# Kernel tuning notes

Measured on AMD Instinct MI355X. Metric: run time of the kernel, lower is better.

## Reference

```python
import math
import jax, jax.numpy as jnp
import numpy as np

B, C, F_, W = 4, 2, 512, 1024
NH = 8
HD = F_ // NH            # 64 head dim
ROT = HD // 2            # 32 rotated dims
NFREQ = ROT // 2         # 16 base freqs ('pixel': linspace(1, max_freq/2, dim//2)*pi)


def mc_linear(x, w_pw):
    # x: [b,c,f_in,w], w_pw: [c, f_out, f_in] -> [b,c,f_out,w]
    return jnp.einsum('bchw,cgh->bcgw', x, w_pw)


def apply_rope(t, freqs):
    # t: [b,c,n,w,d]; freqs: [w, rot_dim] (already pair-repeated)
    rot_dim = freqs.shape[-1]
    t_rot, t_pass = t[..., :rot_dim], t[..., rot_dim:]
    cos, sin = jnp.cos(freqs), jnp.sin(freqs)
    x1, x2 = t_rot[..., 0::2], t_rot[..., 1::2]
    rh = jnp.stack([-x2, x1], axis=-1).reshape(t_rot.shape)  # rotate_half (interleaved pairs)
    return jnp.concatenate([t_rot * cos + rh * sin, t_pass], axis=-1)


def setup_inputs() -> dict:
    key = jax.random.key(0)
    ks = jax.random.split(key, 6)
    x = jax.random.normal(ks[0], (B, C, F_, W), dtype=jnp.float32)
    bound = 1.0 / math.sqrt(F_)
    def w(k):
        return jax.random.uniform(k, (C, F_, F_), minval=-bound, maxval=bound, dtype=jnp.float32)
    wq, wk, wv, wo = w(ks[1]), w(ks[2]), w(ks[3]), w(ks[4])
    # learned 'pixel' freqs: linspace(1., max_freq/2=5., NFREQ) * pi
    freqs_param = (jnp.linspace(1.0, 5.0, NFREQ) * math.pi).astype(jnp.float32)
    return {"x": x, "wq": wq, "wk": wk, "wv": wv, "wo": wo, "freqs_param": freqs_param}


def reference(x, wq, wk, wv, wo, freqs_param):
    b, c, h, w = x.shape
    def heads(t):  # [b,c,h,w] -> [b,c,NH,w,HD]
        return t.transpose(0, 1, 3, 2).reshape(b, c, w, NH, HD).transpose(0, 1, 3, 2, 4)
    pos = jnp.arange(w, dtype=jnp.float32)
    freqs = jnp.repeat(pos[:, None] * freqs_param[None, :], 2, axis=-1)  # [w, ROT]
    # NOTE: original module uses q_proj for q, k, and v (k_proj/v_proj unused)
    q = apply_rope(heads(mc_linear(x, wq)), freqs)
    k = apply_rope(heads(mc_linear(x, wq)), freqs)
    v = heads(mc_linear(x, wq))
    qk = jnp.einsum('bcnqd,bcnkd->bcnqk', q, k) / math.sqrt(h)
    a = jnp.einsum('bcnqk,bcnkd->bcnqd', jax.nn.softmax(qk, axis=-1), v)
    a = a.transpose(0, 1, 3, 2, 4).reshape(b, c, w, NH * HD).transpose(0, 1, 3, 2)  # [b,c,h,w]
    return mc_linear(a, wo)
```

## Files before the change

### kernel.cpp

```cpp
#include <hip/hip_runtime.h>
#include <hip/hip_bf16.h>
#include <math.h>

#define B_ 4
#define C_ 2
#define F_ 512
#define W_ 1024
#define NH_ 8
#define HD_ 64
#define ROT_ 32
#define NFREQ_ 16
#define BC_ (B_*C_)

#define QSC_ 0.2525048f

typedef short bf16x8 __attribute__((ext_vector_type(8)));
typedef float f32x4  __attribute__((ext_vector_type(4)));
typedef float f32x16 __attribute__((ext_vector_type(16)));
typedef unsigned short u16;
typedef unsigned int   u32;

#if __has_builtin(__builtin_amdgcn_exp2f)
#define EXP2(x) __builtin_amdgcn_exp2f(x)
#else
#define EXP2(x) exp2f(x)
#endif

#define VDRAIN() asm volatile("s_waitcnt vmcnt(0)" ::: "memory")

__device__ __forceinline__ u16 f2bf(float f) {
    union { float f; u32 u; } v; v.f = f;
    u32 r = (v.u + 0x7fffu + ((v.u >> 16) & 1u)) >> 16;
    return (u16)r;
}
__device__ __forceinline__ float bf2f(u16 h) {
    union { u32 u; float f; } v; v.u = ((u32)h) << 16;
    return v.f;
}
__device__ __forceinline__ f32x4 mfma16(bf16x8 a, bf16x8 b, f32x4 c) {
    return __builtin_amdgcn_mfma_f32_16x16x32_bf16(a, b, c, 0, 0, 0);
}
__device__ __forceinline__ f32x16 mfma32(bf16x8 a, bf16x8 b, f32x16 c) {
    return __builtin_amdgcn_mfma_f32_32x32x16_bf16(a, b, c, 0, 0, 0);
}
__device__ __forceinline__ void gload16(const u16* g, u16* l) {
    __builtin_amdgcn_global_load_lds(
        (const __attribute__((address_space(1))) u32*)g,
        (__attribute__((address_space(3))) u32*)l, 16, 0, 0);
}
__device__ __forceinline__ u32 pk2(float lo, float hi) {
    __hip_bfloat162 h = __float22bfloat162_rn(make_float2(lo, hi));
    union { __hip_bfloat162 b; u32 u; } cv; cv.b = h; return cv.u;
}
__device__ __forceinline__ void pl32swap(u32& a, u32& b) {
    asm volatile("v_permlane32_swap_b32 %0, %1" : "+v"(a), "+v"(b));
}

__global__ __launch_bounds__(256)
void prep(const float* __restrict__ wq, const float* __restrict__ wo,
          const float* __restrict__ fp,
          u16* __restrict__ wqh, u16* __restrict__ woh, u16* __restrict__ wol,
          float2* __restrict__ trig)
{
    const int b = blockIdx.x, t = threadIdx.x;
    if (b < 512) {
        int i = (b * 256 + t) * 4;
        float4 v = *(const float4*)(wq + i);
        ushort4 h;
        h.x = f2bf(v.x); h.y = f2bf(v.y); h.z = f2bf(v.z); h.w = f2bf(v.w);
        *(ushort4*)(wqh + i) = h;
    } else if (b < 1024) {
        int i = ((b - 512) * 256 + t) * 4;
        float4 v = *(const float4*)(wo + i);
        ushort4 h, l;
        h.x = f2bf(v.x); l.x = f2bf(v.x - bf2f(h.x));
        h.y = f2bf(v.y); l.y = f2bf(v.y - bf2f(h.y));
        h.z = f2bf(v.z); l.z = f2bf(v.z - bf2f(h.z));
        h.w = f2bf(v.w); l.w = f2bf(v.w - bf2f(h.w));
        *(ushort4*)(woh + i) = h;
        *(ushort4*)(wol + i) = l;
    } else {
        int idx = (b - 1024) * 256 + t;
        int w = idx >> 4, j = idx & 15;
        float th = (float)w * fp[j];
        float s, c;
        sincosf(th, &s, &c);
        trig[idx] = make_float2(c, s);
    }
}

__global__ __launch_bounds__(256)
void conv_xt(const float* __restrict__ x, u16* __restrict__ xh) {
    __shared__ float T[64][65];
    const int t = threadIdx.x;
    const int h0 = blockIdx.x * 64, w0 = blockIdx.y * 64, bc = blockIdx.z;
    {
        const int hl = t >> 2, wc = (t & 3) * 16;
        const float* src = x + ((size_t)bc * F_ + h0 + hl) * W_ + w0 + wc;
        #pragma unroll
        for (int z = 0; z < 4; ++z)
            *(float4*)(&T[hl][wc + z * 4]) = *(const float4*)(src + z * 4);
    }
    __syncthreads();
    {
        const int wl = t >> 2, hc = (t & 3) * 16;
        u16 hv[16];
        #pragma unroll
        for (int z = 0; z < 16; ++z) hv[z] = f2bf(T[hc + z][wl]);
        size_t base = ((size_t)bc * W_ + w0 + wl) * F_ + h0 + hc;
        *(uint4*)(xh + base)     = *(uint4*)(hv);
        *(uint4*)(xh + base + 8) = *(uint4*)(hv + 8);
    }
}

template<int MODE>
__global__ __launch_bounds__(256)
void gemm3(const u16* __restrict__ Ah_, const u16* __restrict__ Al_,
           const u16* __restrict__ Bh_, const u16* __restrict__ Bl_,
           u16* __restrict__ Vout, u16* __restrict__ Qout,
           float* __restrict__ Fout, const float2* __restrict__ trig)
{
    constexpr int BUFS = MODE ? 16384 : 8192;
    __shared__ u16 sh[2 * BUFS];

    const int tid = threadIdx.x, lane = tid & 63, wid = tid >> 6;
    const int m0 = blockIdx.x * 128, n0 = blockIdx.y * 128, bc = blockIdx.z, c = bc % C_;
    const u16* Abh = Ah_ + (size_t)c * F_ * F_;
    const u16* Abl = MODE ? (Al_ + (size_t)c * F_ * F_) : (const u16*)nullptr;
    const u16* Bbh = Bh_ + (size_t)bc * W_ * F_;
    const u16* Bbl = MODE ? (Bl_ + (size_t)bc * W_ * F_) : (const u16*)nullptr;

    f32x4 acc[4][4] = {};
    const int mb = (wid >> 1) * 64, nb = (wid & 1) * 64;
    const int r_in = lane >> 2, tsl = lane & 3;

    auto STAGE = [&](int k0, int buf) {
        u16* base = sh + buf * BUFS;
        #pragma unroll
        for (int h = 0; h < 2; ++h) {
            const int row = h * 64 + wid * 16 + r_in;
            const int ts  = tsl ^ ((row >> 1) & 3);
            const int lb  = (h * 64 + wid * 16) * 32;
            gload16(Abh + (size_t)(m0 + row) * F_ + k0 + ts * 8, base + lb);
            gload16(Bbh + (size_t)(n0 + row) * F_ + k0 + ts * 8, base + 4096 + lb);
            if constexpr (MODE) {
                gload16(Abl + (size_t)(m0 + row) * F_ + k0 + ts * 8, base + 8192 + lb);
                gload16(Bbl + (size_t)(n0 + row) * F_ + k0 + ts * 8, base + 12288 + lb);
            }
        }
    };

    STAGE(0, 0);
    VDRAIN();
    __syncthreads();
    int cur = 0;
    for (int kt = 0; kt < 16; ++kt) {
        if (kt < 15) STAGE((kt + 1) * 32, cur ^ 1);
        const u16* Ash = sh + cur * BUFS;
        const u16* Bsh = Ash + 4096;
        const u16* Asl = MODE ? Ash + 8192  : Ash;
        const u16* Bsl = MODE ? Ash + 12288 : Ash;

        bf16x8 fah[4], fal[4];
        #pragma unroll
        for (int i = 0; i < 4; ++i) {
            const int row = mb + i * 16 + (lane & 15);
            const int idx = row * 32 + (((lane >> 4) ^ ((row >> 1) & 3)) << 3);
            fah[i] = *(const bf16x8*)(&Ash[idx]);
            if constexpr (MODE) fal[i] = *(const bf16x8*)(&Asl[idx]);
        }
        #pragma unroll
        for (int j = 0; j < 4; ++j) {
            const int rowb = nb + j * 16 + (lane & 15);
            const int idxb = rowb * 32 + (((lane >> 4) ^ ((rowb >> 1) & 3)) << 3);
            bf16x8 bh = *(const bf16x8*)(&Bsh[idxb]);
            #pragma unroll
            for (int i = 0; i < 4; ++i)
                acc[i][j] = mfma16(fah[i], bh, acc[i][j]);
            if constexpr (MODE) {
                bf16x8 bl = *(const bf16x8*)(&Bsl[idxb]);
                #pragma unroll
                for (int i = 0; i < 4; ++i) {
                    acc[i][j] = mfma16(fah[i], bl, acc[i][j]);
                    acc[i][j] = mfma16(fal[i], bh, acc[i][j]);
                }
            }
        }
        VDRAIN();
        __syncthreads();
        cur ^= 1;
    }

    #pragma unroll
    for (int i = 0; i < 4; ++i) {
        const int gr = m0 + mb + i * 16 + (lane >> 4) * 4;
        #pragma unroll
        for (int j = 0; j < 4; ++j) {
            const int wc = n0 + nb + j * 16 + (lane & 15);
            #pragma unroll
            for (int r = 0; r < 4; ++r) {
                const size_t ad = ((size_t)bc * F_ + gr + r) * W_ + wc;
                if constexpr (MODE == 1) Fout[ad] = acc[i][j][r];
                else                     Vout[ad] = f2bf(acc[i][j][r]);
            }
        }
    }

    if constexpr (MODE == 0) {
        __syncthreads();
        u16* Qt = sh + wid * 4096;
        #pragma unroll
        for (int j = 0; j < 4; ++j) {
            const int wl = j * 16 + (lane & 15);
            const int wg = n0 + nb + wl;
            #pragma unroll
            for (int i = 0; i < 4; ++i) {
                const int ddb = i * 16 + (lane >> 4) * 4;
                float q[4];
                if (i < 2) {
                    #pragma unroll
                    for (int p = 0; p < 2; ++p) {
                        const int fidx = (ddb >> 1) + p;
                        float2 cs = trig[wg * NFREQ_ + fidx];
                        float e = acc[i][j][2 * p], o = acc[i][j][2 * p + 1];
                        q[2 * p]     = (e * cs.x - o * cs.y) * QSC_;
                        q[2 * p + 1] = (o * cs.x + e * cs.y) * QSC_;
                    }
                } else {
                    #pragma unroll
                    for (int r = 0; r < 4; ++r) q[r] = acc[i][j][r] * QSC_;
                }
                #pragma unroll
                for (int r = 0; r < 4; ++r)
                    Qt[wl * 64 + ((ddb + r) ^ ((wl & 7) << 3))] = f2bf(q[r]);
            }
        }
        const int wl = lane;
        const int wg = n0 + nb + wl;
        const int head = (m0 + mb) >> 6;
        const size_t qbase = (((size_t)bc * NH_ + head) * W_ + wg) * 64;
        #pragma unroll
        for (int s = 0; s < 8; ++s) {
            uint4 v = *(const uint4*)(&Qt[wl * 64 + ((s ^ (wl & 7)) << 3)]);
            *(uint4*)(&Qout[qbase + s * 8]) = v;
        }
    }
}

__global__ __launch_bounds__(256)
void attn3(const u16* __restrict__ Qt, const u16* __restrict__ Vg,
           u16* __restrict__ Ah, u16* __restrict__ Al)
{
    __shared__ u16 sh[16384];
    const int tid = threadIdx.x, lane = tid & 63, wid = tid >> 6;
    const int q0 = blockIdx.x * 128, head = blockIdx.y, bc = blockIdx.z;
    const u16* qb = Qt + ((size_t)bc * NH_ + head) * W_ * 64;
    const u16* vb = Vg + ((size_t)bc * F_ + head * HD_) * W_;

    const int qcol = lane & 31, hi = lane >> 5;
    const int srow = lane >> 3, st = lane & 7;

    bf16x8 qf[4];
    {
        const u16* qrow = qb + (size_t)(q0 + wid * 32 + qcol) * 64 + hi * 8;
        #pragma unroll
        for (int ks = 0; ks < 4; ++ks)
            qf[ks] = *(const bf16x8*)(qrow + ks * 16);
    }

    f32x16 o0, o1;
    #pragma unroll
    for (int i = 0; i < 16; ++i) { o0[i] = 0.f; o1[i] = 0.f; }
    float lsum = 0.f;

    auto STAGE = [&](int kt, int buf) {
        const int k0 = kt * 64;
        u16* Ksb = sh + buf * 8192;
        u16* Vsb = Ksb + 4096;
        #pragma unroll
        for (int p = 0; p < 2; ++p) {
            const int rb = wid * 16 + p * 8;
            const int r  = rb + srow;
            const int ts = st ^ (r & 7);
            gload16(qb + (size_t)(k0 + r) * 64 + ts * 8, Ksb + rb * 64);
            gload16(vb + (size_t)r * W_ + k0 + ts * 8,   Vsb + rb * 64);
        }
    };

    STAGE(0, 0);
    VDRAIN();
    __syncthreads();
    int cur = 0;
    for (int kt = 0; kt < 16; ++kt) {
        if (kt < 15) STAGE(kt + 1, cur ^ 1);
        const u16* Ks = sh + cur * 8192;
        const u16* Vs = Ks + 4096;

        f32x16 s0, s1;
        #pragma unroll
        for (int i = 0; i < 16; ++i) { s0[i] = 0.f; s1[i] = 0.f; }
        #pragma unroll
        for (int ks = 0; ks < 4; ++ks) {
            const int sl = ks * 2 + hi;
            const int kA = qcol;
            const int kB = 32 + qcol;
            bf16x8 kf0 = *(const bf16x8*)(Ks + kA * 64 + ((sl ^ (kA & 7)) << 3));
            bf16x8 kf1 = *(const bf16x8*)(Ks + kB * 64 + ((sl ^ (kB & 7)) << 3));
            s0 = mfma32(kf0, qf[ks], s0);
            s1 = mfma32(kf1, qf[ks], s1);
        }

        float p0[16], p1[16];
        #pragma unroll
        for (int i = 0; i < 16; ++i) { p0[i] = EXP2(s0[i]); p1[i] = EXP2(s1[i]); }
        float part = 0.f;
        #pragma unroll
        for (int i = 0; i < 16; ++i) part += p0[i] + p1[i];
        lsum += part;

        bf16x8 pf[4];
        #pragma unroll
        for (int kb = 0; kb < 2; ++kb) {
            const float* pp = kb ? p1 : p0;
            #pragma unroll
            for (int f = 0; f < 2; ++f) {
                u32 a1 = pk2(pp[f*8+0], pp[f*8+1]);
                u32 a2 = pk2(pp[f*8+2], pp[f*8+3]);
                u32 b1 = pk2(pp[f*8+4], pp[f*8+5]);
                u32 b2 = pk2(pp[f*8+6], pp[f*8+7]);
                pl32swap(a1, b1);
                pl32swap(a2, b2);
                union { u32 w[4]; bf16x8 v; } u;
                u.w[0] = a1; u.w[1] = a2; u.w[2] = b1; u.w[3] = b2;
                pf[kb * 2 + f] = u.v;
            }
        }

        #pragma unroll
        for (int ks2 = 0; ks2 < 4; ++ks2) {
            const int sl = ks2 * 2 + hi;
            const int d0r = qcol;
            const int d1r = 32 + qcol;
            bf16x8 vf0 = *(const bf16x8*)(Vs + d0r * 64 + ((sl ^ (d0r & 7)) << 3));
            bf16x8 vf1 = *(const bf16x8*)(Vs + d1r * 64 + ((sl ^ (d1r & 7)) << 3));
            o0 = mfma32(vf0, pf[ks2], o0);
            o1 = mfma32(vf1, pf[ks2], o1);
        }
        VDRAIN();
        __syncthreads();
        cur ^= 1;
    }

    lsum += __shfl_xor(lsum, 32);
    const float inv = 1.f / lsum;

    const int wrow = q0 + wid * 32 + qcol;
    const size_t rowbase = ((size_t)bc * W_ + wrow) * F_ + head * HD_;
    #pragma unroll
    for (int dblk = 0; dblk < 2; ++dblk) {
        const f32x16 ov = dblk ? o1 : o0;
        const int coloff = dblk * 32;
        #pragma unroll
        for (int pr = 0; pr < 8; ++pr) {
            const float v1 = ov[2 * pr]     * inv;
            const float v2 = ov[2 * pr + 1] * inv;
            const int drow = ((2 * pr) & 3) + 8 * (pr >> 1) + 4 * hi;
            const u16 h1 = f2bf(v1), h2 = f2bf(v2);
            const u16 l1 = f2bf(v1 - bf2f(h1)), l2 = f2bf(v2 - bf2f(h2));
            *(u32*)(Ah + rowbase + coloff + drow) = (u32)h1 | ((u32)h2 << 16);
            *(u32*)(Al + rowbase + coloff + drow) = (u32)l1 | ((u32)l2 << 16);
        }
    }
}

extern "C" void kernel_launch(void* const* d_in, const int* in_sizes, int n_in,
                              void* d_out, int out_size, void* d_ws, size_t ws_size,
                              hipStream_t stream) {
    const float* x  = (const float*)d_in[0];
    const float* wq = (const float*)d_in[1];
    const float* wo = (const float*)d_in[4];
    const float* fp = (const float*)d_in[5];
    float* out = (float*)d_out;

    char* w8 = (char*)d_ws;
    const size_t MB = 1024 * 1024;
    u16* xh   = (u16*)(w8);
    u16* wqh  = (u16*)(w8 + 8 * MB);
    u16* woh  = (u16*)(w8 + 9 * MB);
    u16* wol  = (u16*)(w8 + 10 * MB);
    float2* trig = (float2*)(w8 + 11 * MB);
    u16* qbuf = (u16*)(w8 + 12 * MB);
    u16* vbuf = (u16*)(w8 + 20 * MB);
    u16* al   = (u16*)(w8 + 28 * MB);
    u16* ah   = xh;

    prep<<<1088, 256, 0, stream>>>(wq, wo, fp, wqh, woh, wol, trig);
    conv_xt<<<dim3(F_ / 64, W_ / 64, BC_), 256, 0, stream>>>(x, xh);

    gemm3<0><<<dim3(F_ / 128, W_ / 128, BC_), 256, 0, stream>>>(
        wqh, nullptr, xh, nullptr, vbuf, qbuf, nullptr, trig);

    attn3<<<dim3(W_ / 128, NH_, BC_), 256, 0, stream>>>(qbuf, vbuf, ah, al);

    gemm3<1><<<dim3(F_ / 128, W_ / 128, BC_), 256, 0, stream>>>(
        woh, wol, ah, al, nullptr, nullptr, out, nullptr);
}
```

Measured before the change: 148.6 us.

## Fuse prep with x transpose and halve GEMM M-tile to fill more CUs

Merges the weight/trig prep kernel and the x transpose-convert kernel into one launch, which removes a kernel launch boundary. It also shrinks the GEMM block tile from 128x128 to 64x128. That doubles the grid from 256 to 512 blocks so the many CUs on MI355X are better occupied. The cost is lower per-block data reuse, with more loads of the B operand per FLOP. The Q epilogue is reworked so each block writes one head, with the half-head (rotated or pass-through) chosen per wave row.

```diff
diff --git a/kernel.cpp b/kernel.cpp
--- a/kernel.cpp
+++ b/kernel.cpp
@@ -57,11 +57,12 @@
 }
 
 __global__ __launch_bounds__(256)
-void prep(const float* __restrict__ wq, const float* __restrict__ wo,
-          const float* __restrict__ fp,
-          u16* __restrict__ wqh, u16* __restrict__ woh, u16* __restrict__ wol,
-          float2* __restrict__ trig)
+void prep_all(const float* __restrict__ wq, const float* __restrict__ wo,
+              const float* __restrict__ fp, const float* __restrict__ x,
+              u16* __restrict__ wqh, u16* __restrict__ woh, u16* __restrict__ wol,
+              float2* __restrict__ trig, u16* __restrict__ xh)
 {
+    __shared__ float T[64][65];
     const int b = blockIdx.x, t = threadIdx.x;
     if (b < 512) {
         int i = (b * 256 + t) * 4;
@@ -79,74 +80,72 @@
         h.w = f2bf(v.w); l.w = f2bf(v.w - bf2f(h.w));
         *(ushort4*)(woh + i) = h;
         *(ushort4*)(wol + i) = l;
-    } else {
+    } else if (b < 1088) {
         int idx = (b - 1024) * 256 + t;
         int w = idx >> 4, j = idx & 15;
         float th = (float)w * fp[j];
         float s, c;
         sincosf(th, &s, &c);
         trig[idx] = make_float2(c, s);
-    }
-}
-
-__global__ __launch_bounds__(256)
-void conv_xt(const float* __restrict__ x, u16* __restrict__ xh) {
-    __shared__ float T[64][65];
-    const int t = threadIdx.x;
-    const int h0 = blockIdx.x * 64, w0 = blockIdx.y * 64, bc = blockIdx.z;
-    {
-        const int hl = t >> 2, wc = (t & 3) * 16;
-        const float* src = x + ((size_t)bc * F_ + h0 + hl) * W_ + w0 + wc;
-        #pragma unroll
-        for (int z = 0; z < 4; ++z)
-            *(float4*)(&T[hl][wc + z * 4]) = *(const float4*)(src + z * 4);
-    }
-    __syncthreads();
-    {
-        const int wl = t >> 2, hc = (t & 3) * 16;
-        u16 hv[16];
-        #pragma unroll
-        for (int z = 0; z < 16; ++z) hv[z] = f2bf(T[hc + z][wl]);
-        size_t base = ((size_t)bc * W_ + w0 + wl) * F_ + h0 + hc;
-        *(uint4*)(xh + base)     = *(uint4*)(hv);
-        *(uint4*)(xh + base + 8) = *(uint4*)(hv + 8);
+    } else {
+        const int b2 = b - 1088;
+        const int h0 = (b2 & 7) * 64, w0 = ((b2 >> 3) & 15) * 64, bc = b2 >> 7;
+        {
+            const int hl = t >> 2, wc = (t & 3) * 16;
+            const float* src = x + ((size_t)bc * F_ + h0 + hl) * W_ + w0 + wc;
+            #pragma unroll
+            for (int z = 0; z < 4; ++z)
+                *(float4*)(&T[hl][wc + z * 4]) = *(const float4*)(src + z * 4);
+        }
+        __syncthreads();
+        {
+            const int wl = t >> 2, hc = (t & 3) * 16;
+            u16 hv[16];
+            #pragma unroll
+            for (int z = 0; z < 16; ++z) hv[z] = f2bf(T[hc + z][wl]);
+            size_t base = ((size_t)bc * W_ + w0 + wl) * F_ + h0 + hc;
+            *(uint4*)(xh + base)     = *(uint4*)(hv);
+            *(uint4*)(xh + base + 8) = *(uint4*)(hv + 8);
+        }
     }
 }
 
 template<int MODE>
 __global__ __launch_bounds__(256)
-void gemm3(const u16* __restrict__ Ah_, const u16* __restrict__ Al_,
+void gemm4(const u16* __restrict__ Ah_, const u16* __restrict__ Al_,
            const u16* __restrict__ Bh_, const u16* __restrict__ Bl_,
            u16* __restrict__ Vout, u16* __restrict__ Qout,
            float* __restrict__ Fout, const float2* __restrict__ trig)
 {
-    constexpr int BUFS = MODE ? 16384 : 8192;
+    constexpr int BUFS = MODE ? 12288 : 6144;
     __shared__ u16 sh[2 * BUFS];
 
     const int tid = threadIdx.x, lane = tid & 63, wid = tid >> 6;
-    const int m0 = blockIdx.x * 128, n0 = blockIdx.y * 128, bc = blockIdx.z, c = bc % C_;
+    const int wm = wid >> 1, wn = wid & 1;
+    const int m0 = blockIdx.x * 64, n0 = blockIdx.y * 128, bc = blockIdx.z, c = bc % C_;
     const u16* Abh = Ah_ + (size_t)c * F_ * F_;
     const u16* Abl = MODE ? (Al_ + (size_t)c * F_ * F_) : (const u16*)nullptr;
     const u16* Bbh = Bh_ + (size_t)bc * W_ * F_;
     const u16* Bbl = MODE ? (Bl_ + (size_t)bc * W_ * F_) : (const u16*)nullptr;
 
-    f32x4 acc[4][4] = {};
-    const int mb = (wid >> 1) * 64, nb = (wid & 1) * 64;
-    const int r_in = lane >> 2, tsl = lane & 3;
+    f32x4 acc[2][4] = {};
+    const int srow = tid >> 2, sslot = tid & 3;
 
     auto STAGE = [&](int k0, int buf) {
         u16* base = sh + buf * BUFS;
+        {
+            const int ts = sslot ^ ((srow >> 1) & 3);
+            const size_t ga = (size_t)(m0 + srow) * F_ + k0 + ts * 8;
+            gload16(Abh + ga, base + wid * 512);
+            if constexpr (MODE) gload16(Abl + ga, base + 6144 + wid * 512);
+        }
         #pragma unroll
         for (int h = 0; h < 2; ++h) {
-            const int row = h * 64 + wid * 16 + r_in;
-            const int ts  = tsl ^ ((row >> 1) & 3);
-            const int lb  = (h * 64 + wid * 16) * 32;
-            gload16(Abh + (size_t)(m0 + row) * F_ + k0 + ts * 8, base + lb);
-            gload16(Bbh + (size_t)(n0 + row) * F_ + k0 + ts * 8, base + 4096 + lb);
-            if constexpr (MODE) {
-                gload16(Abl + (size_t)(m0 + row) * F_ + k0 + ts * 8, base + 8192 + lb);
-                gload16(Bbl + (size_t)(n0 + row) * F_ + k0 + ts * 8, base + 12288 + lb);
-            }
+            const int brow = h * 64 + srow;
+            const int ts = sslot ^ ((brow >> 1) & 3);
+            const size_t gb = (size_t)(n0 + brow) * F_ + k0 + ts * 8;
+            gload16(Bbh + gb, base + 2048 + h * 2048 + wid * 512);
+            if constexpr (MODE) gload16(Bbl + gb, base + 8192 + h * 2048 + wid * 512);
         }
     };
 
@@ -157,30 +156,30 @@
     for (int kt = 0; kt < 16; ++kt) {
         if (kt < 15) STAGE((kt + 1) * 32, cur ^ 1);
         const u16* Ash = sh + cur * BUFS;
-        const u16* Bsh = Ash + 4096;
-        const u16* Asl = MODE ? Ash + 8192  : Ash;
-        const u16* Bsl = MODE ? Ash + 12288 : Ash;
-
-        bf16x8 fah[4], fal[4];
-        #pragma unroll
-        for (int i = 0; i < 4; ++i) {
-            const int row = mb + i * 16 + (lane & 15);
+        const u16* Bsh = Ash + 2048;
+        const u16* Asl = Ash + 6144;
+        const u16* Bsl = Ash + 8192;
+
+        bf16x8 fah[2], fal[2];
+        #pragma unroll
+        for (int i = 0; i < 2; ++i) {
+            const int row = wm * 32 + i * 16 + (lane & 15);
             const int idx = row * 32 + (((lane >> 4) ^ ((row >> 1) & 3)) << 3);
             fah[i] = *(const bf16x8*)(&Ash[idx]);
             if constexpr (MODE) fal[i] = *(const bf16x8*)(&Asl[idx]);
         }
         #pragma unroll
         for (int j = 0; j < 4; ++j) {
-            const int rowb = nb + j * 16 + (lane & 15);
+            const int rowb = wn * 64 + j * 16 + (lane & 15);
             const int idxb = rowb * 32 + (((lane >> 4) ^ ((rowb >> 1) & 3)) << 3);
             bf16x8 bh = *(const bf16x8*)(&Bsh[idxb]);
             #pragma unroll
-            for (int i = 0; i < 4; ++i)
+            for (int i = 0; i < 2; ++i)
                 acc[i][j] = mfma16(fah[i], bh, acc[i][j]);
             if constexpr (MODE) {
                 bf16x8 bl = *(const bf16x8*)(&Bsl[idxb]);
                 #pragma unroll
-                for (int i = 0; i < 4; ++i) {
+                for (int i = 0; i < 2; ++i) {
                     acc[i][j] = mfma16(fah[i], bl, acc[i][j]);
                     acc[i][j] = mfma16(fal[i], bh, acc[i][j]);
                 }
@@ -192,11 +191,11 @@
     }
 
     #pragma unroll
-    for (int i = 0; i < 4; ++i) {
-        const int gr = m0 + mb + i * 16 + (lane >> 4) * 4;
+    for (int i = 0; i < 2; ++i) {
+        const int gr = m0 + wm * 32 + i * 16 + (lane >> 4) * 4;
         #pragma unroll
         for (int j = 0; j < 4; ++j) {
-            const int wc = n0 + nb + j * 16 + (lane & 15);
+            const int wc = n0 + wn * 64 + j * 16 + (lane & 15);
             #pragma unroll
             for (int r = 0; r < 4; ++r) {
                 const size_t ad = ((size_t)bc * F_ + gr + r) * W_ + wc;
@@ -208,19 +207,19 @@
 
     if constexpr (MODE == 0) {
         __syncthreads();
-        u16* Qt = sh + wid * 4096;
+        u16* Qt = sh + wid * 2048;
+        const int head = blockIdx.x;
         #pragma unroll
         for (int j = 0; j < 4; ++j) {
             const int wl = j * 16 + (lane & 15);
-            const int wg = n0 + nb + wl;
-            #pragma unroll
-            for (int i = 0; i < 4; ++i) {
-                const int ddb = i * 16 + (lane >> 4) * 4;
+            const int wg = n0 + wn * 64 + wl;
+            #pragma unroll
+            for (int i = 0; i < 2; ++i) {
                 float q[4];
-                if (i < 2) {
+                if (wm == 0) {
                     #pragma unroll
                     for (int p = 0; p < 2; ++p) {
-                        const int fidx = (ddb >> 1) + p;
+                        const int fidx = i * 8 + (lane >> 4) * 2 + p;
                         float2 cs = trig[wg * NFREQ_ + fidx];
                         float e = acc[i][j][2 * p], o = acc[i][j][2 * p + 1];
                         q[2 * p]     = (e * cs.x - o * cs.y) * QSC_;
@@ -231,18 +230,17 @@
                     for (int r = 0; r < 4; ++r) q[r] = acc[i][j][r] * QSC_;
                 }
                 #pragma unroll
-                for (int r = 0; r < 4; ++r)
-                    Qt[wl * 64 + ((ddb + r) ^ ((wl & 7) << 3))] = f2bf(q[r]);
+                for (int r = 0; r < 4; ++r) {
+                    const int ddl = i * 16 + (lane >> 4) * 4 + r;
+                    Qt[wl * 32 + ((ddl & 7) | (((ddl >> 3) ^ (wl & 3)) << 3))] = f2bf(q[r]);
+                }
             }
         }
-        const int wl = lane;
-        const int wg = n0 + nb + wl;
-        const int head = (m0 + mb) >> 6;
-        const size_t qbase = (((size_t)bc * NH_ + head) * W_ + wg) * 64;
-        #pragma unroll
-        for (int s = 0; s < 8; ++s) {
-            uint4 v = *(const uint4*)(&Qt[wl * 64 + ((s ^ (wl & 7)) << 3)]);
-            *(uint4*)(&Qout[qbase + s * 8]) = v;
+        const size_t qrow = (((size_t)bc * NH_ + head) * W_ + n0 + wn * 64 + lane) * 64 + wm * 32;
+        #pragma unroll
+        for (int s = 0; s < 4; ++s) {
+            uint4 v = *(const uint4*)(&Qt[lane * 32 + ((s ^ (lane & 3)) << 3)]);
+            *(uint4*)(&Qout[qrow + s * 8]) = v;
         }
     }
 }
@@ -394,14 +392,13 @@
     u16* al   = (u16*)(w8 + 28 * MB);
     u16* ah   = xh;
 
-    prep<<<1088, 256, 0, stream>>>(wq, wo, fp, wqh, woh, wol, trig);
-    conv_xt<<<dim3(F_ / 64, W_ / 64, BC_), 256, 0, stream>>>(x, xh);
-
-    gemm3<0><<<dim3(F_ / 128, W_ / 128, BC_), 256, 0, stream>>>(
+    prep_all<<<2112, 256, 0, stream>>>(wq, wo, fp, x, wqh, woh, wol, trig, xh);
+
+    gemm4<0><<<dim3(8, 8, 8), 256, 0, stream>>>(
         wqh, nullptr, xh, nullptr, vbuf, qbuf, nullptr, trig);
 
     attn3<<<dim3(W_ / 128, NH_, BC_), 256, 0, stream>>>(qbuf, vbuf, ah, al);
 
-    gemm3<1><<<dim3(F_ / 128, W_ / 128, BC_), 256, 0, stream>>>(
+    gemm4<1><<<dim3(8, 8, 8), 256, 0, stream>>>(
         woh, wol, ah, al, nullptr, nullptr, out, nullptr);
 }
```

New measurement: 150.8 us. No clear change (+1.5%).
